# Optimization experiments

Measured on AMD Instinct MI355X. Metric: run time of the kernel, lower is better.

## Reference

```python
import jax, jax.numpy as jnp
import numpy as np

D, HS, HE, E, K = 1024, 2048, 1024, 8, 2   # d_model, shared hidden (d_ff//2), expert hidden (d_ff//4), n_experts, top_k
B, T = 4, 1024
N_SHARED = 1


def setup_inputs() -> dict:
    key = jax.random.key(0)
    ks = jax.random.split(key, 9)
    g = lambda k, shape, s: jax.random.normal(k, shape, jnp.float32) * s
    return {
        "x": g(ks[0], (B, T, D), 1.0),
        "t_emb": g(ks[1], (B, D), 1.0),
        "router_W": g(ks[2], (2 * D, E), 0.01),      # torch Linear(2C->E, bias=False), std=0.01 init
        "router_bias": jnp.zeros((E,), jnp.float32),  # load-balance bias buffer
        "w1": g(ks[3], (D, HS), 0.02),                # shared expert SwiGLU
        "w3": g(ks[4], (D, HS), 0.02),
        "w2": g(ks[5], (HS, D), 0.02),
        "W1e": g(ks[6], (E, D, HE), 0.02),            # routed experts, Linear->GELU->Linear
        "W2e": g(ks[7], (E, HE, D), 0.02),
    }


def reference(x, t_emb, router_W, router_bias, w1, w3, w2, W1e, W2e):
    Bb, Tt, C = x.shape
    xf = x.reshape(-1, C)                                              # [N, C]
    tf = jnp.broadcast_to(t_emb[:, None, :], (Bb, Tt, C)).reshape(-1, C)
    N = xf.shape[0]

    shared = (jax.nn.silu(xf @ w1) * (xf @ w3)) @ w2                   # [N, C]

    # router affinity (sigmoid, fp32)
    s = jax.nn.sigmoid((jnp.concatenate([xf, tf], axis=-1) @ router_W).astype(jnp.float32))
    sel_scores = s + router_bias                                       # [N, E]
    _, topk_idx = jax.lax.top_k(sel_scores, K)                         # [N, K]

    # gates normalized over selected raw affinities
    s_sel = jnp.take_along_axis(s, topk_idx, axis=1)                   # [N, K]
    denom = s_sel.sum(axis=1, keepdims=True)
    gates = jnp.where(denom > 1e-9, s_sel / (denom + 1e-9), 1.0 / K).astype(x.dtype)

    # combine weights [N, E]: scatter gates to selected experts
    combine = jnp.zeros((N, E), x.dtype).at[jnp.arange(N)[:, None], topk_idx].add(gates)

    # dense expert evaluation (reference form of grouped GEMM + scatter-combine)
    h = jax.nn.gelu(jnp.einsum('nc,ech->enh', xf, W1e), approximate=False)  # [E, N, He]
    y = jnp.einsum('enh,ehc->enc', h, W2e)                                   # [E, N, C]
    routed = jnp.einsum('ne,enc->nc', combine, y)                            # [N, C]

    return ((shared + routed) / (N_SHARED + K)).reshape(Bb, Tt, C)
```

## Files before the change

### kernel.cpp

```cpp
#include <hip/hip_runtime.h>
#include <hip/hip_bf16.h>
#include <math.h>

#define D_MODEL 1024
#define HS 2048
#define HE 1024
#define NEXP 8
#define NTOK 4096
#define NSLOT 8192

typedef __attribute__((ext_vector_type(4))) float f32x4;
typedef __attribute__((ext_vector_type(8))) short bf16x8;

__device__ __forceinline__ short f2b(float f) {
  __hip_bfloat16 h = __float2bfloat16(f);
  return *reinterpret_cast<short*>(&h);
}
__device__ __forceinline__ float b2f(short s) {
  return __bfloat162float(*reinterpret_cast<__hip_bfloat16*>(&s));
}

__device__ __forceinline__ void gl_lds16(const short* g, short* l) {
  __builtin_amdgcn_global_load_lds(
      (const __attribute__((address_space(1))) void*)g,
      (__attribute__((address_space(3))) void*)l, 16, 0, 0);
}

__device__ __forceinline__ void tr_tile(const float* __restrict__ in,
                                        short* __restrict__ out, int R, int C,
                                        int bx, int by, int bz, int rmap,
                                        float (*tile)[69], int t) {
  const int c0 = bx * 64;
  const int r0 = by * 64;
  const size_t bo = (size_t)bz * R * C;
  const int lr = t >> 4;
  const int lc4 = (t & 15) * 4;
#pragma unroll
  for (int i = 0; i < 4; i++) {
    const float4 v = *(const float4*)&in[bo + (size_t)(r0 + lr + i * 16) * C + c0 + lc4];
    tile[lc4 + 0][lr + i * 16] = v.x;
    tile[lc4 + 1][lr + i * 16] = v.y;
    tile[lc4 + 2][lr + i * 16] = v.z;
    tile[lc4 + 3][lr + i * 16] = v.w;
  }
  __syncthreads();
#pragma unroll
  for (int i = 0; i < 4; i++) {
    const int oc = (t >> 4) + i * 16;
    const int or4 = (t & 15) * 4;
    short4 o;
    o.x = f2b(tile[oc][or4 + 0]);
    o.y = f2b(tile[oc][or4 + 1]);
    o.z = f2b(tile[oc][or4 + 2]);
    o.w = f2b(tile[oc][or4 + 3]);
    const int c = c0 + oc;
    size_t orow;
    if (rmap == 0) orow = bo + (size_t)c * R;
    else orow = (size_t)((c >> 5) * 64 + (rmap == 2 ? 32 : 0) + (c & 31)) * R;
    *(short4*)&out[orow + r0 + or4] = o;
  }
}

__global__ __launch_bounds__(256) void tr_w13(const float* __restrict__ w1,
                                              const float* __restrict__ w3,
                                              short* __restrict__ w13I) {
  __shared__ float tile[64][69];
  const int z = blockIdx.z;
  tr_tile(z ? w3 : w1, w13I, D_MODEL, HS, blockIdx.x, blockIdx.y, 0, z ? 2 : 1,
          tile, threadIdx.x);
}

__global__ __launch_bounds__(256) void tr_w2(const float* __restrict__ w2,
                                             short* __restrict__ w2T) {
  __shared__ float tile[64][69];
  tr_tile(w2, w2T, HS, D_MODEL, blockIdx.x, blockIdx.y, 0, 0, tile, threadIdx.x);
}

__global__ __launch_bounds__(256) void tr_exp(const float* __restrict__ W1e,
                                              const float* __restrict__ W2e,
                                              short* __restrict__ W1eT,
                                              short* __restrict__ W2eT) {
  __shared__ float tile[64][69];
  const int z = blockIdx.z;
  if (z < 8)
    tr_tile(W1e, W1eT, D_MODEL, HE, blockIdx.x, blockIdx.y, z, 0, tile, threadIdx.x);
  else
    tr_tile(W2e, W2eT, HE, D_MODEL, blockIdx.x, blockIdx.y, z - 8, 0, tile, threadIdx.x);
}

__global__ __launch_bounds__(256) void router_kernel(
    const float* __restrict__ x, const float* __restrict__ temb,
    const float* __restrict__ rw, const float* __restrict__ rbias,
    short* __restrict__ xb, int* __restrict__ topk, float* __restrict__ gates) {
  const int t = (blockIdx.x * 256 + threadIdx.x) >> 6;
  const int lane = threadIdx.x & 63;
  const float* xr = x + (size_t)t * D_MODEL;
  const float* tr = temb + (size_t)(t >> 10) * D_MODEL;
  float acc[NEXP] = {};
#pragma unroll
  for (int i = 0; i < 4; i++) {
    const int j = i * 256 + lane * 4;
    const float4 xv = *(const float4*)&xr[j];
    const float4 tv = *(const float4*)&tr[j];
    short4 o;
    o.x = f2b(xv.x); o.y = f2b(xv.y); o.z = f2b(xv.z); o.w = f2b(xv.w);
    *(short4*)&xb[(size_t)t * D_MODEL + j] = o;
    const float* wx = rw + (size_t)j * NEXP;
    const float* wt = rw + (size_t)(D_MODEL + j) * NEXP;
    const float xa[4] = {xv.x, xv.y, xv.z, xv.w};
    const float ta[4] = {tv.x, tv.y, tv.z, tv.w};
#pragma unroll
    for (int u = 0; u < 4; u++)
#pragma unroll
      for (int e = 0; e < NEXP; e++)
        acc[e] += xa[u] * wx[u * NEXP + e] + ta[u] * wt[u * NEXP + e];
  }
#pragma unroll
  for (int off = 32; off; off >>= 1)
#pragma unroll
    for (int e = 0; e < NEXP; e++) acc[e] += __shfl_xor(acc[e], off);
  if (lane == 0) {
    float s[NEXP], sel[NEXP];
#pragma unroll
    for (int e = 0; e < NEXP; e++) {
      s[e] = 1.f / (1.f + expf(-acc[e]));
      sel[e] = s[e] + rbias[e];
    }
    int i0 = 0;
#pragma unroll
    for (int e = 1; e < NEXP; e++) if (sel[e] > sel[i0]) i0 = e;
    int i1 = (i0 == 0) ? 1 : 0;
#pragma unroll
    for (int e = 0; e < NEXP; e++) if (e != i0 && sel[e] > sel[i1]) i1 = e;
    float s0 = s[i0], s1 = s[i1], den = s0 + s1;
    float g0, g1;
    if (den > 1e-9f) { g0 = s0 / (den + 1e-9f); g1 = s1 / (den + 1e-9f); }
    else { g0 = 0.5f; g1 = 0.5f; }
    topk[t * 2] = i0; topk[t * 2 + 1] = i1;
    gates[t * 2] = g0; gates[t * 2 + 1] = g1;
  }
}

__global__ __launch_bounds__(1024) void group_kernel(const int* __restrict__ topk,
                                                     int* __restrict__ perm,
                                                     int* __restrict__ offs,
                                                     int* __restrict__ te,
                                                     int* __restrict__ tm,
                                                     int* __restrict__ ntile) {
  __shared__ int cnt[NEXP], cur[NEXP];
  const int t = threadIdx.x;
  if (t < NEXP) cnt[t] = 0;
  __syncthreads();
  int mye[8];
#pragma unroll
  for (int i = 0; i < 8; i++) {
    mye[i] = topk[i * 1024 + t];
    atomicAdd(&cnt[mye[i]], 1);
  }
  __syncthreads();
  if (t == 0) {
    int a = 0;
    for (int e = 0; e < NEXP; e++) { offs[e] = a; cur[e] = a; a += cnt[e]; }
    offs[NEXP] = a;
    int nt = 0;
    for (int e = 0; e < NEXP; e++)
      for (int m0 = 0; m0 < cnt[e]; m0 += 256) { te[nt] = e; tm[nt] = m0; nt++; }
    ntile[0] = nt;
  }
  __syncthreads();
#pragma unroll
  for (int i = 0; i < 8; i++) {
    int pos = atomicAdd(&cur[mye[i]], 1);
    perm[pos] = i * 1024 + t;
  }
}

template <int MODE>
__global__ __launch_bounds__(512, 1) void moe_gemm_ct(
    const short* __restrict__ A, const short* __restrict__ B, short* __restrict__ Cout,
    const int* __restrict__ perm, const int* __restrict__ offs,
    const float* __restrict__ gates, const int* __restrict__ te,
    const int* __restrict__ tm, const int* __restrict__ ntile) {
  extern __shared__ short lds[];
  const int td = threadIdx.x;
  int bx, m0, rbeg = 0, rend = 0;
  const short* Bbase;
  if (MODE == 0) {
    const int id = blockIdx.x, xcd = id & 7, slot = id >> 3;
    bx = (xcd & 3) * 4 + (slot & 3);
    m0 = ((xcd >> 2) * 8 + (slot >> 2)) * 256;
    Bbase = B + (size_t)bx * 256 * 1024;
  } else {
    const int id = blockIdx.x;
    const int work = (id & 7) * 20 + (id >> 3);
    const int ty = work >> 2;
    if (ty >= ntile[0]) return;
    bx = work & 3;
    const int e = te[ty];
    m0 = tm[ty];
    rbeg = offs[e]; rend = offs[e + 1];
    Bbase = B + ((size_t)e * 1024 + bx * 256) * 1024;
  }

  const int srow = td >> 3;
  const int colsw8 = ((td & 7) ^ (srow & 7)) * 8;
  const short* ap[2][2];
  const short* bp[2][2];
#pragma unroll
  for (int h = 0; h < 2; h++)
#pragma unroll
    for (int i = 0; i < 2; i++) {
      const int trow = h * 128 + i * 64 + srow;
      int grow;
      if (MODE == 0) grow = m0 + trow;
      else if (MODE == 1) grow = perm[min(rbeg + m0 + trow, rend - 1)] >> 1;
      else grow = min(rbeg + m0 + trow, rend - 1);
      ap[h][i] = A + (size_t)grow * 1024 + colsw8;
      bp[h][i] = Bbase + (size_t)trow * 1024 + colsw8;
    }

#define STAGE_ALL(t_, b_)                                                       \
  do {                                                                          \
    gl_lds16(bp[0][0] + (t_) * 64, lds + (b_) * 32768 + 16384 + td * 8);        \
    gl_lds16(bp[0][1] + (t_) * 64, lds + (b_) * 32768 + 16384 + 4096 + td * 8); \
    gl_lds16(bp[1][0] + (t_) * 64, lds + (b_) * 32768 + 16384 + 8192 + td * 8); \
    gl_lds16(bp[1][1] + (t_) * 64, lds + (b_) * 32768 + 16384 + 12288 + td * 8);\
    gl_lds16(ap[0][0] + (t_) * 64, lds + (b_) * 32768 + td * 8);                \
    gl_lds16(ap[0][1] + (t_) * 64, lds + (b_) * 32768 + 4096 + td * 8);         \
    gl_lds16(ap[1][0] + (t_) * 64, lds + (b_) * 32768 + 8192 + td * 8);         \
    gl_lds16(ap[1][1] + (t_) * 64, lds + (b_) * 32768 + 12288 + td * 8);        \
  } while (0)

  const int l = td & 63;
  const int wid = td >> 6;
  const int mh = wid >> 2;
  const int wn4 = wid & 3;
  const int lr = l & 15;
  const int bhsel = wn4 >> 1;
  const int bnr = (wn4 & 1) * 64;
  const int swzk0 = ((0 + (l >> 4) * 16) ^ ((l & 7) << 4)) >> 1;
  const int swzk1 = ((64 + (l >> 4) * 16) ^ ((l & 7) << 4)) >> 1;

#define LDA(mf_, swz_) (*(const bf16x8*)&Ah[(unsigned)(((mf_)*16 + lr) * 64) + (swz_)])
#define LDB(nf_, swz_) (*(const bf16x8*)&Bh[(unsigned)((bnr + (nf_)*16 + lr) * 64) + (swz_)])
#define MMROW(mf_, a_)                                                                 \
  acc[mf_][0] = __builtin_amdgcn_mfma_f32_16x16x32_bf16(a_, b0, acc[mf_][0], 0, 0, 0); \
  acc[mf_][1] = __builtin_amdgcn_mfma_f32_16x16x32_bf16(a_, b1, acc[mf_][1], 0, 0, 0); \
  acc[mf_][2] = __builtin_amdgcn_mfma_f32_16x16x32_bf16(a_, b2, acc[mf_][2], 0, 0, 0); \
  acc[mf_][3] = __builtin_amdgcn_mfma_f32_16x16x32_bf16(a_, b3, acc[mf_][3], 0, 0, 0)

  f32x4 acc[8][4] = {};

  STAGE_ALL(0, 0);

  for (int t = 0; t < 16; ++t) {
    const int p = t & 1, q = p ^ 1;
    const short* Ah = lds + p * 32768 + mh * 8192;
    const short* Bh = lds + p * 32768 + 16384 + bhsel * 8192;
    if (t < 15) {
      STAGE_ALL(t + 1, q);
      asm volatile("s_waitcnt vmcnt(8)" ::: "memory");
    } else {
      asm volatile("s_waitcnt vmcnt(0)" ::: "memory");
    }
    __builtin_amdgcn_s_barrier();
    {
      bf16x8 b0, b1, b2, b3, a0, a1, a2, a3;
      b0 = LDB(0, swzk0); b1 = LDB(1, swzk0); b2 = LDB(2, swzk0); b3 = LDB(3, swzk0);
      a0 = LDA(0, swzk0); a1 = LDA(1, swzk0); a2 = LDA(2, swzk0); a3 = LDA(3, swzk0);
      __builtin_amdgcn_s_setprio(1);
      MMROW(0, a0); MMROW(1, a1); MMROW(2, a2); MMROW(3, a3);
      __builtin_amdgcn_s_setprio(0);
      a0 = LDA(4, swzk0); a1 = LDA(5, swzk0); a2 = LDA(6, swzk0); a3 = LDA(7, swzk0);
      __builtin_amdgcn_s_setprio(1);
      MMROW(4, a0); MMROW(5, a1); MMROW(6, a2); MMROW(7, a3);
      __builtin_amdgcn_s_setprio(0);
      b0 = LDB(0, swzk1); b1 = LDB(1, swzk1); b2 = LDB(2, swzk1); b3 = LDB(3, swzk1);
      a0 = LDA(0, swzk1); a1 = LDA(1, swzk1); a2 = LDA(2, swzk1); a3 = LDA(3, swzk1);
      __builtin_amdgcn_s_setprio(1);
      MMROW(0, a0); MMROW(1, a1); MMROW(2, a2); MMROW(3, a3);
      __builtin_amdgcn_s_setprio(0);
      a0 = LDA(4, swzk1); a1 = LDA(5, swzk1); a2 = LDA(6, swzk1); a3 = LDA(7, swzk1);
      __builtin_amdgcn_s_setprio(1);
      MMROW(4, a0); MMROW(5, a1); MMROW(6, a2); MMROW(7, a3);
      __builtin_amdgcn_s_setprio(0);
    }
    __builtin_amdgcn_sched_barrier(0);
    __builtin_amdgcn_s_barrier();
  }

  const int rsub = (l >> 4) * 4;
  if (MODE == 0) {
#pragma unroll
    for (int mf = 0; mf < 8; mf++)
#pragma unroll
      for (int j = 0; j < 4; j++) {
        const int row = m0 + mh * 128 + mf * 16 + rsub + j;
        short* Up = Cout + (size_t)row * HS + bx * 128 + wn4 * 32 + lr;
#pragma unroll
        for (int nfp = 0; nfp < 2; nfp++) {
          const float a = acc[mf][nfp][j];
          const float b = acc[mf][nfp + 2][j];
          Up[nfp * 16] = f2b(a / (1.f + expf(-a)) * b);
        }
      }
  } else if (MODE == 1) {
#pragma unroll
    for (int mf = 0; mf < 8; mf++)
#pragma unroll
      for (int j = 0; j < 4; j++) {
        const int gi = rbeg + m0 + mh * 128 + mf * 16 + rsub + j;
        if (gi < rend) {
          short* Cp = Cout + (size_t)gi * HE + bx * 256 + wn4 * 64 + lr;
#pragma unroll
          for (int nf = 0; nf < 4; nf++) {
            const float v = acc[mf][nf][j];
            Cp[nf * 16] = f2b(0.5f * v * (1.0f + erff(v * 0.70710678118654752f)));
          }
        }
      }
  } else {
#pragma unroll
    for (int mf = 0; mf < 8; mf++)
#pragma unroll
      for (int j = 0; j < 4; j++) {
        const int gi = rbeg + m0 + mh * 128 + mf * 16 + rsub + j;
        if (gi < rend) {
          const int slot = perm[gi];
          const float g = gates[slot];
          short* Cp = Cout + (size_t)slot * D_MODEL + bx * 256 + wn4 * 64 + lr;
#pragma unroll
          for (int nf = 0; nf < 4; nf++) Cp[nf * 16] = f2b(g * acc[mf][nf][j]);
        }
      }
  }
#undef STAGE_ALL
#undef LDA
#undef LDB
#undef MMROW
}

__global__ __launch_bounds__(256, 2) void gemm_g2_ct(
    const short* __restrict__ A, const short* __restrict__ B,
    const short* __restrict__ yb, float* __restrict__ out) {
  extern __shared__ short lds[];
  const int td = threadIdx.x;
  const int id = blockIdx.x, xcd = id & 7, slot = id >> 3;
  const int tile_n = (slot & 7) * 128;
  const int m0 = (xcd * 4 + (slot >> 3)) * 128;

  const int srow = td >> 3;
  const int colsw8 = ((td & 7) ^ (srow & 7)) * 8;
  const short* ap[4];
  const short* bp[4];
#pragma unroll
  for (int u = 0; u < 4; u++) {
    ap[u] = A + (size_t)(m0 + u * 32 + srow) * HS + colsw8;
    bp[u] = B + (size_t)(tile_n + u * 32 + srow) * HS + colsw8;
  }

#define STAGE_ALL2(t_, b_)                                                 \
  do {                                                                     \
    gl_lds16(ap[0] + (t_) * 64, lds + (b_) * 16384 + td * 8);              \
    gl_lds16(ap[1] + (t_) * 64, lds + (b_) * 16384 + 2048 + td * 8);       \
    gl_lds16(ap[2] + (t_) * 64, lds + (b_) * 16384 + 4096 + td * 8);       \
    gl_lds16(ap[3] + (t_) * 64, lds + (b_) * 16384 + 6144 + td * 8);       \
    gl_lds16(bp[0] + (t_) * 64, lds + (b_) * 16384 + 8192 + td * 8);       \
    gl_lds16(bp[1] + (t_) * 64, lds + (b_) * 16384 + 10240 + td * 8);      \
    gl_lds16(bp[2] + (t_) * 64, lds + (b_) * 16384 + 12288 + td * 8);      \
    gl_lds16(bp[3] + (t_) * 64, lds + (b_) * 16384 + 14336 + td * 8);      \
  } while (0)

  const int l = td & 63;
  const int wv = td >> 6;
  const int wm = (wv >> 1) * 64, wn = (wv & 1) * 64;
  const int lr = l & 15;
  const int swzk0 = ((0 + (l >> 4) * 16) ^ ((l & 7) << 4)) >> 1;
  const int swzk1 = ((64 + (l >> 4) * 16) ^ ((l & 7) << 4)) >> 1;

#define LDA2(mf_, swz_) (*(const bf16x8*)&Ah[(unsigned)(((mf_)*16 + lr) * 64) + (swz_)])
#define LDB2(nf_, swz_) (*(const bf16x8*)&Bh[(unsigned)(((nf_)*16 + lr) * 64) + (swz_)])
#define MMROW2(mf_, a_)                                                                \
  acc[mf_][0] = __builtin_amdgcn_mfma_f32_16x16x32_bf16(a_, b0, acc[mf_][0], 0, 0, 0); \
  acc[mf_][1] = __builtin_amdgcn_mfma_f32_16x16x32_bf16(a_, b1, acc[mf_][1], 0, 0, 0); \
  acc[mf_][2] = __builtin_amdgcn_mfma_f32_16x16x32_bf16(a_, b2, acc[mf_][2], 0, 0, 0); \
  acc[mf_][3] = __builtin_amdgcn_mfma_f32_16x16x32_bf16(a_, b3, acc[mf_][3], 0, 0, 0)

  f32x4 acc[4][4] = {};

  STAGE_ALL2(0, 0);
  for (int t = 0; t < 32; ++t) {
    const int p = t & 1, q = p ^ 1;
    const short* Ah = lds + p * 16384 + wm * 64;
    const short* Bh = lds + p * 16384 + 8192 + wn * 64;
    if (t < 31) {
      STAGE_ALL2(t + 1, q);
      asm volatile("s_waitcnt vmcnt(8)" ::: "memory");
    } else {
      asm volatile("s_waitcnt vmcnt(0)" ::: "memory");
    }
    __builtin_amdgcn_s_barrier();
    {
      bf16x8 b0, b1, b2, b3, a0, a1, a2, a3;
      b0 = LDB2(0, swzk0); b1 = LDB2(1, swzk0); b2 = LDB2(2, swzk0); b3 = LDB2(3, swzk0);
      a0 = LDA2(0, swzk0); a1 = LDA2(1, swzk0); a2 = LDA2(2, swzk0); a3 = LDA2(3, swzk0);
      __builtin_amdgcn_s_setprio(1);
      MMROW2(0, a0); MMROW2(1, a1); MMROW2(2, a2); MMROW2(3, a3);
      __builtin_amdgcn_s_setprio(0);
      b0 = LDB2(0, swzk1); b1 = LDB2(1, swzk1); b2 = LDB2(2, swzk1); b3 = LDB2(3, swzk1);
      a0 = LDA2(0, swzk1); a1 = LDA2(1, swzk1); a2 = LDA2(2, swzk1); a3 = LDA2(3, swzk1);
      __builtin_amdgcn_s_setprio(1);
      MMROW2(0, a0); MMROW2(1, a1); MMROW2(2, a2); MMROW2(3, a3);
      __builtin_amdgcn_s_setprio(0);
    }
    __builtin_amdgcn_sched_barrier(0);
    __builtin_amdgcn_s_barrier();
  }

  const int rq = (l >> 4) * 4;
  const float inv3 = 1.0f / 3.0f;
#pragma unroll
  for (int m = 0; m < 4; m++) {
#pragma unroll
    for (int j = 0; j < 4; j++) {
      const int tok = m0 + wm + m * 16 + rq + j;
      const int colb = tile_n + wn + lr;
      const short* y0p = yb + (size_t)(tok * 2) * D_MODEL + colb;
      const short* y1p = yb + (size_t)(tok * 2 + 1) * D_MODEL + colb;
      float* Op = out + (size_t)tok * D_MODEL + colb;
#pragma unroll
      for (int n = 0; n < 4; n++) {
        Op[n * 16] = (acc[m][n][j] + b2f(y0p[n * 16]) + b2f(y1p[n * 16])) * inv3;
      }
    }
  }
#undef STAGE_ALL2
#undef LDA2
#undef LDB2
#undef MMROW2
}

extern "C" void kernel_launch(void* const* d_in, const int* in_sizes, int n_in,
                              void* d_out, int out_size, void* d_ws, size_t ws_size,
                              hipStream_t stream) {
  const float* x = (const float*)d_in[0];
  const float* temb = (const float*)d_in[1];
  const float* rw = (const float*)d_in[2];
  const float* rbias = (const float*)d_in[3];
  const float* w1 = (const float*)d_in[4];
  const float* w3 = (const float*)d_in[5];
  const float* w2 = (const float*)d_in[6];
  const float* W1e = (const float*)d_in[7];
  const float* W2e = (const float*)d_in[8];
  float* out = (float*)d_out;

  const size_t MB = 1ull << 20;
  char* w = (char*)d_ws;
  short* xb    = (short*)(w + 0 * MB);
  short* w13I  = (short*)(w + 8 * MB);
  short* w2T   = (short*)(w + 16 * MB);
  short* W1eT  = (short*)(w + 20 * MB);
  short* W2eT  = (short*)(w + 36 * MB);
  short* ubuf  = (short*)(w + 52 * MB);
  short* hexpb = (short*)(w + 68 * MB);
  short* yb    = (short*)(w + 84 * MB);
  float* gates = (float*)(w + 100 * MB);
  int* topk    = (int*)(w + 100 * MB + 32 * 1024);
  int* perm    = (int*)(w + 100 * MB + 64 * 1024);
  int* meta    = (int*)(w + 100 * MB + 96 * 1024);
  int* offs    = meta;
  int* te      = meta + 16;
  int* tm      = meta + 128;
  int* ntile   = meta + 256;

  hipFuncSetAttribute((const void*)&moe_gemm_ct<0>,
                      hipFuncAttributeMaxDynamicSharedMemorySize, 131072);
  hipFuncSetAttribute((const void*)&moe_gemm_ct<1>,
                      hipFuncAttributeMaxDynamicSharedMemorySize, 131072);
  hipFuncSetAttribute((const void*)&moe_gemm_ct<2>,
                      hipFuncAttributeMaxDynamicSharedMemorySize, 131072);
  hipFuncSetAttribute((const void*)&gemm_g2_ct,
                      hipFuncAttributeMaxDynamicSharedMemorySize, 65536);

  tr_w13<<<dim3(HS / 64, D_MODEL / 64, 2), 256, 0, stream>>>(w1, w3, w13I);
  tr_w2<<<dim3(D_MODEL / 64, HS / 64, 1), 256, 0, stream>>>(w2, w2T);
  tr_exp<<<dim3(16, 16, 16), 256, 0, stream>>>(W1e, W2e, W1eT, W2eT);
  router_kernel<<<NTOK / 4, 256, 0, stream>>>(x, temb, rw, rbias, xb, topk, gates);
  group_kernel<<<1, 1024, 0, stream>>>(topk, perm, offs, te, tm, ntile);

  moe_gemm_ct<0><<<256, 512, 131072, stream>>>(xb, w13I, ubuf, nullptr, nullptr,
                                               nullptr, nullptr, nullptr, nullptr);

  moe_gemm_ct<1><<<160, 512, 131072, stream>>>(xb, W1eT, hexpb, perm, offs,
                                               gates, te, tm, ntile);
  moe_gemm_ct<2><<<160, 512, 131072, stream>>>(hexpb, W2eT, yb, perm, offs,
                                               gates, te, tm, ntile);

  gemm_g2_ct<<<256, 256, 65536, stream>>>(ubuf, w2T, yb, out);
}
```

Baseline: 225.7 us.

## Switch MoE and shared GEMMs to unified 128x128 tile kernel with two blocks per CU

Replaces the 256x256-tile, 512-thread GEMM used for the shared up-projection and both routed-expert GEMMs with a templated 128x128-tile, 256-thread kernel at two blocks per CU. The down-projection kernel is folded into the same template. Expert grouping now emits 128-row tiles, which cuts padding waste on uneven expert loads and gives more blocks for better CU fill. The trade is less operand reuse per tile, so each block does more global and LDS traffic per FLOP.

```diff
diff --git a/kernel.cpp b/kernel.cpp
--- a/kernel.cpp
+++ b/kernel.cpp
@@ -164,7 +164,7 @@
     offs[NEXP] = a;
     int nt = 0;
     for (int e = 0; e < NEXP; e++)
-      for (int m0 = 0; m0 < cnt[e]; m0 += 256) { te[nt] = e; tm[nt] = m0; nt++; }
+      for (int m0 = 0; m0 < cnt[e]; m0 += 128) { te[nt] = e; tm[nt] = m0; nt++; }
     ntile[0] = nt;
   }
   __syncthreads();
@@ -175,90 +175,91 @@
   }
 }
 
-template <int MODE>
-__global__ __launch_bounds__(512, 1) void moe_gemm_ct(
-    const short* __restrict__ A, const short* __restrict__ B, short* __restrict__ Cout,
+template <int MODE, int NT>
+__global__ __launch_bounds__(256, 2) void g128(
+    const short* __restrict__ A, const short* __restrict__ B, void* __restrict__ Cout,
     const int* __restrict__ perm, const int* __restrict__ offs,
     const float* __restrict__ gates, const int* __restrict__ te,
-    const int* __restrict__ tm, const int* __restrict__ ntile) {
+    const int* __restrict__ tm, const int* __restrict__ ntile,
+    const short* __restrict__ yb) {
   extern __shared__ short lds[];
   const int td = threadIdx.x;
-  int bx, m0, rbeg = 0, rend = 0;
+  const int K = NT * 64;
+
+  int m_panel = 0, n_panel = 0, e = 0, m0 = 0, rbeg = 0, rend = 0, bxn = 0;
   const short* Bbase;
   if (MODE == 0) {
-    const int id = blockIdx.x, xcd = id & 7, slot = id >> 3;
-    bx = (xcd & 3) * 4 + (slot & 3);
-    m0 = ((xcd >> 2) * 8 + (slot >> 2)) * 256;
-    Bbase = B + (size_t)bx * 256 * 1024;
+    const int xcd = blockIdx.x & 7, w = blockIdx.x >> 3;
+    n_panel = xcd * 4 + (w >> 5);
+    m_panel = w & 31;
+    Bbase = B + (size_t)n_panel * 128 * K;
+  } else if (MODE == 3) {
+    const int xcd = blockIdx.x & 7, slot = blockIdx.x >> 3;
+    n_panel = slot & 7;
+    m_panel = xcd * 4 + (slot >> 3);
+    Bbase = B + (size_t)n_panel * 128 * K;
   } else {
-    const int id = blockIdx.x;
-    const int work = (id & 7) * 20 + (id >> 3);
-    const int ty = work >> 2;
+    const int ty = blockIdx.x >> 3;
     if (ty >= ntile[0]) return;
-    bx = work & 3;
-    const int e = te[ty];
+    bxn = blockIdx.x & 7;
+    e = te[ty];
     m0 = tm[ty];
     rbeg = offs[e]; rend = offs[e + 1];
-    Bbase = B + ((size_t)e * 1024 + bx * 256) * 1024;
+    Bbase = B + ((size_t)e * 1024 + bxn * 128) * K;
   }
 
   const int srow = td >> 3;
   const int colsw8 = ((td & 7) ^ (srow & 7)) * 8;
-  const short* ap[2][2];
-  const short* bp[2][2];
-#pragma unroll
-  for (int h = 0; h < 2; h++)
-#pragma unroll
-    for (int i = 0; i < 2; i++) {
-      const int trow = h * 128 + i * 64 + srow;
-      int grow;
-      if (MODE == 0) grow = m0 + trow;
-      else if (MODE == 1) grow = perm[min(rbeg + m0 + trow, rend - 1)] >> 1;
-      else grow = min(rbeg + m0 + trow, rend - 1);
-      ap[h][i] = A + (size_t)grow * 1024 + colsw8;
-      bp[h][i] = Bbase + (size_t)trow * 1024 + colsw8;
-    }
-
-#define STAGE_ALL(t_, b_)                                                       \
-  do {                                                                          \
-    gl_lds16(bp[0][0] + (t_) * 64, lds + (b_) * 32768 + 16384 + td * 8);        \
-    gl_lds16(bp[0][1] + (t_) * 64, lds + (b_) * 32768 + 16384 + 4096 + td * 8); \
-    gl_lds16(bp[1][0] + (t_) * 64, lds + (b_) * 32768 + 16384 + 8192 + td * 8); \
-    gl_lds16(bp[1][1] + (t_) * 64, lds + (b_) * 32768 + 16384 + 12288 + td * 8);\
-    gl_lds16(ap[0][0] + (t_) * 64, lds + (b_) * 32768 + td * 8);                \
-    gl_lds16(ap[0][1] + (t_) * 64, lds + (b_) * 32768 + 4096 + td * 8);         \
-    gl_lds16(ap[1][0] + (t_) * 64, lds + (b_) * 32768 + 8192 + td * 8);         \
-    gl_lds16(ap[1][1] + (t_) * 64, lds + (b_) * 32768 + 12288 + td * 8);        \
+  const short* ap[4];
+  const short* bp[4];
+#pragma unroll
+  for (int u = 0; u < 4; u++) {
+    const int trow = u * 32 + srow;
+    int grow;
+    if (MODE == 0) grow = m_panel * 128 + trow;
+    else if (MODE == 1) grow = perm[min(rbeg + m0 + trow, rend - 1)] >> 1;
+    else if (MODE == 2) grow = min(rbeg + m0 + trow, rend - 1);
+    else grow = m_panel * 128 + trow;
+    ap[u] = A + (size_t)grow * K + colsw8;
+    bp[u] = Bbase + (size_t)trow * K + colsw8;
+  }
+
+#define STAGE(t_, b_)                                                      \
+  do {                                                                     \
+    gl_lds16(ap[0] + (t_) * 64, lds + (b_) * 16384 + td * 8);              \
+    gl_lds16(ap[1] + (t_) * 64, lds + (b_) * 16384 + 2048 + td * 8);       \
+    gl_lds16(ap[2] + (t_) * 64, lds + (b_) * 16384 + 4096 + td * 8);       \
+    gl_lds16(ap[3] + (t_) * 64, lds + (b_) * 16384 + 6144 + td * 8);       \
+    gl_lds16(bp[0] + (t_) * 64, lds + (b_) * 16384 + 8192 + td * 8);       \
+    gl_lds16(bp[1] + (t_) * 64, lds + (b_) * 16384 + 10240 + td * 8);      \
+    gl_lds16(bp[2] + (t_) * 64, lds + (b_) * 16384 + 12288 + td * 8);      \
+    gl_lds16(bp[3] + (t_) * 64, lds + (b_) * 16384 + 14336 + td * 8);      \
   } while (0)
 
   const int l = td & 63;
-  const int wid = td >> 6;
-  const int mh = wid >> 2;
-  const int wn4 = wid & 3;
+  const int wv = td >> 6;
+  const int wm = (wv >> 1) * 64, wn = (wv & 1) * 64;
   const int lr = l & 15;
-  const int bhsel = wn4 >> 1;
-  const int bnr = (wn4 & 1) * 64;
   const int swzk0 = ((0 + (l >> 4) * 16) ^ ((l & 7) << 4)) >> 1;
   const int swzk1 = ((64 + (l >> 4) * 16) ^ ((l & 7) << 4)) >> 1;
 
 #define LDA(mf_, swz_) (*(const bf16x8*)&Ah[(unsigned)(((mf_)*16 + lr) * 64) + (swz_)])
-#define LDB(nf_, swz_) (*(const bf16x8*)&Bh[(unsigned)((bnr + (nf_)*16 + lr) * 64) + (swz_)])
+#define LDB(nf_, swz_) (*(const bf16x8*)&Bh[(unsigned)(((nf_)*16 + lr) * 64) + (swz_)])
 #define MMROW(mf_, a_)                                                                 \
   acc[mf_][0] = __builtin_amdgcn_mfma_f32_16x16x32_bf16(a_, b0, acc[mf_][0], 0, 0, 0); \
   acc[mf_][1] = __builtin_amdgcn_mfma_f32_16x16x32_bf16(a_, b1, acc[mf_][1], 0, 0, 0); \
   acc[mf_][2] = __builtin_amdgcn_mfma_f32_16x16x32_bf16(a_, b2, acc[mf_][2], 0, 0, 0); \
   acc[mf_][3] = __builtin_amdgcn_mfma_f32_16x16x32_bf16(a_, b3, acc[mf_][3], 0, 0, 0)
 
-  f32x4 acc[8][4] = {};
-
-  STAGE_ALL(0, 0);
-
-  for (int t = 0; t < 16; ++t) {
+  f32x4 acc[4][4] = {};
+
+  STAGE(0, 0);
+  for (int t = 0; t < NT; ++t) {
     const int p = t & 1, q = p ^ 1;
-    const short* Ah = lds + p * 32768 + mh * 8192;
-    const short* Bh = lds + p * 32768 + 16384 + bhsel * 8192;
-    if (t < 15) {
-      STAGE_ALL(t + 1, q);
+    const short* Ah = lds + p * 16384 + wm * 64;
+    const short* Bh = lds + p * 16384 + 8192 + wn * 64;
+    if (t < NT - 1) {
+      STAGE(t + 1, q);
       asm volatile("s_waitcnt vmcnt(8)" ::: "memory");
     } else {
       asm volatile("s_waitcnt vmcnt(0)" ::: "memory");
@@ -271,47 +272,39 @@
       __builtin_amdgcn_s_setprio(1);
       MMROW(0, a0); MMROW(1, a1); MMROW(2, a2); MMROW(3, a3);
       __builtin_amdgcn_s_setprio(0);
-      a0 = LDA(4, swzk0); a1 = LDA(5, swzk0); a2 = LDA(6, swzk0); a3 = LDA(7, swzk0);
-      __builtin_amdgcn_s_setprio(1);
-      MMROW(4, a0); MMROW(5, a1); MMROW(6, a2); MMROW(7, a3);
-      __builtin_amdgcn_s_setprio(0);
       b0 = LDB(0, swzk1); b1 = LDB(1, swzk1); b2 = LDB(2, swzk1); b3 = LDB(3, swzk1);
       a0 = LDA(0, swzk1); a1 = LDA(1, swzk1); a2 = LDA(2, swzk1); a3 = LDA(3, swzk1);
       __builtin_amdgcn_s_setprio(1);
       MMROW(0, a0); MMROW(1, a1); MMROW(2, a2); MMROW(3, a3);
       __builtin_amdgcn_s_setprio(0);
-      a0 = LDA(4, swzk1); a1 = LDA(5, swzk1); a2 = LDA(6, swzk1); a3 = LDA(7, swzk1);
-      __builtin_amdgcn_s_setprio(1);
-      MMROW(4, a0); MMROW(5, a1); MMROW(6, a2); MMROW(7, a3);
-      __builtin_amdgcn_s_setprio(0);
     }
     __builtin_amdgcn_sched_barrier(0);
     __builtin_amdgcn_s_barrier();
   }
 
-  const int rsub = (l >> 4) * 4;
+  const int rq = (l >> 4) * 4;
   if (MODE == 0) {
 #pragma unroll
-    for (int mf = 0; mf < 8; mf++)
+    for (int mf = 0; mf < 4; mf++)
 #pragma unroll
       for (int j = 0; j < 4; j++) {
-        const int row = m0 + mh * 128 + mf * 16 + rsub + j;
-        short* Up = Cout + (size_t)row * HS + bx * 128 + wn4 * 32 + lr;
-#pragma unroll
-        for (int nfp = 0; nfp < 2; nfp++) {
-          const float a = acc[mf][nfp][j];
-          const float b = acc[mf][nfp + 2][j];
-          Up[nfp * 16] = f2b(a / (1.f + expf(-a)) * b);
+        const int row = m_panel * 128 + wm + mf * 16 + rq + j;
+        short* Up = (short*)Cout + (size_t)row * HS + n_panel * 64 + (wn >> 1) + lr;
+#pragma unroll
+        for (int nf = 0; nf < 2; nf++) {
+          const float a = acc[mf][nf][j];
+          const float b = acc[mf][nf + 2][j];
+          Up[nf * 16] = f2b(a / (1.f + expf(-a)) * b);
         }
       }
   } else if (MODE == 1) {
 #pragma unroll
-    for (int mf = 0; mf < 8; mf++)
+    for (int mf = 0; mf < 4; mf++)
 #pragma unroll
       for (int j = 0; j < 4; j++) {
-        const int gi = rbeg + m0 + mh * 128 + mf * 16 + rsub + j;
+        const int gi = rbeg + m0 + wm + mf * 16 + rq + j;
         if (gi < rend) {
-          short* Cp = Cout + (size_t)gi * HE + bx * 256 + wn4 * 64 + lr;
+          short* Cp = (short*)Cout + (size_t)gi * HE + bxn * 128 + wn + lr;
 #pragma unroll
           for (int nf = 0; nf < 4; nf++) {
             const float v = acc[mf][nf][j];
@@ -319,125 +312,41 @@
           }
         }
       }
-  } else {
-#pragma unroll
-    for (int mf = 0; mf < 8; mf++)
+  } else if (MODE == 2) {
+#pragma unroll
+    for (int mf = 0; mf < 4; mf++)
 #pragma unroll
       for (int j = 0; j < 4; j++) {
-        const int gi = rbeg + m0 + mh * 128 + mf * 16 + rsub + j;
+        const int gi = rbeg + m0 + wm + mf * 16 + rq + j;
         if (gi < rend) {
           const int slot = perm[gi];
           const float g = gates[slot];
-          short* Cp = Cout + (size_t)slot * D_MODEL + bx * 256 + wn4 * 64 + lr;
+          short* Cp = (short*)Cout + (size_t)slot * D_MODEL + bxn * 128 + wn + lr;
 #pragma unroll
           for (int nf = 0; nf < 4; nf++) Cp[nf * 16] = f2b(g * acc[mf][nf][j]);
         }
       }
-  }
-#undef STAGE_ALL
+  } else {
+    const float inv3 = 1.0f / 3.0f;
+#pragma unroll
+    for (int mf = 0; mf < 4; mf++)
+#pragma unroll
+      for (int j = 0; j < 4; j++) {
+        const int tok = m_panel * 128 + wm + mf * 16 + rq + j;
+        const int colb = n_panel * 128 + wn + lr;
+        const short* y0p = yb + (size_t)(tok * 2) * D_MODEL + colb;
+        const short* y1p = yb + (size_t)(tok * 2 + 1) * D_MODEL + colb;
+        float* Op = (float*)Cout + (size_t)tok * D_MODEL + colb;
+#pragma unroll
+        for (int nf = 0; nf < 4; nf++) {
+          Op[nf * 16] = (acc[mf][nf][j] + b2f(y0p[nf * 16]) + b2f(y1p[nf * 16])) * inv3;
+        }
+      }
+  }
+#undef STAGE
 #undef LDA
 #undef LDB
 #undef MMROW
-}
-
-__global__ __launch_bounds__(256, 2) void gemm_g2_ct(
-    const short* __restrict__ A, const short* __restrict__ B,
-    const short* __restrict__ yb, float* __restrict__ out) {
-  extern __shared__ short lds[];
-  const int td = threadIdx.x;
-  const int id = blockIdx.x, xcd = id & 7, slot = id >> 3;
-  const int tile_n = (slot & 7) * 128;
-  const int m0 = (xcd * 4 + (slot >> 3)) * 128;
-
-  const int srow = td >> 3;
-  const int colsw8 = ((td & 7) ^ (srow & 7)) * 8;
-  const short* ap[4];
-  const short* bp[4];
-#pragma unroll
-  for (int u = 0; u < 4; u++) {
-    ap[u] = A + (size_t)(m0 + u * 32 + srow) * HS + colsw8;
-    bp[u] = B + (size_t)(tile_n + u * 32 + srow) * HS + colsw8;
-  }
-
-#define STAGE_ALL2(t_, b_)                                                 \
-  do {                                                                     \
-    gl_lds16(ap[0] + (t_) * 64, lds + (b_) * 16384 + td * 8);              \
-    gl_lds16(ap[1] + (t_) * 64, lds + (b_) * 16384 + 2048 + td * 8);       \
-    gl_lds16(ap[2] + (t_) * 64, lds + (b_) * 16384 + 4096 + td * 8);       \
-    gl_lds16(ap[3] + (t_) * 64, lds + (b_) * 16384 + 6144 + td * 8);       \
-    gl_lds16(bp[0] + (t_) * 64, lds + (b_) * 16384 + 8192 + td * 8);       \
-    gl_lds16(bp[1] + (t_) * 64, lds + (b_) * 16384 + 10240 + td * 8);      \
-    gl_lds16(bp[2] + (t_) * 64, lds + (b_) * 16384 + 12288 + td * 8);      \
-    gl_lds16(bp[3] + (t_) * 64, lds + (b_) * 16384 + 14336 + td * 8);      \
-  } while (0)
-
-  const int l = td & 63;
-  const int wv = td >> 6;
-  const int wm = (wv >> 1) * 64, wn = (wv & 1) * 64;
-  const int lr = l & 15;
-  const int swzk0 = ((0 + (l >> 4) * 16) ^ ((l & 7) << 4)) >> 1;
-  const int swzk1 = ((64 + (l >> 4) * 16) ^ ((l & 7) << 4)) >> 1;
-
-#define LDA2(mf_, swz_) (*(const bf16x8*)&Ah[(unsigned)(((mf_)*16 + lr) * 64) + (swz_)])
-#define LDB2(nf_, swz_) (*(const bf16x8*)&Bh[(unsigned)(((nf_)*16 + lr) * 64) + (swz_)])
-#define MMROW2(mf_, a_)                                                                \
-  acc[mf_][0] = __builtin_amdgcn_mfma_f32_16x16x32_bf16(a_, b0, acc[mf_][0], 0, 0, 0); \
-  acc[mf_][1] = __builtin_amdgcn_mfma_f32_16x16x32_bf16(a_, b1, acc[mf_][1], 0, 0, 0); \
-  acc[mf_][2] = __builtin_amdgcn_mfma_f32_16x16x32_bf16(a_, b2, acc[mf_][2], 0, 0, 0); \
-  acc[mf_][3] = __builtin_amdgcn_mfma_f32_16x16x32_bf16(a_, b3, acc[mf_][3], 0, 0, 0)
-
-  f32x4 acc[4][4] = {};
-
-  STAGE_ALL2(0, 0);
-  for (int t = 0; t < 32; ++t) {
-    const int p = t & 1, q = p ^ 1;
-    const short* Ah = lds + p * 16384 + wm * 64;
-    const short* Bh = lds + p * 16384 + 8192 + wn * 64;
-    if (t < 31) {
-      STAGE_ALL2(t + 1, q);
-      asm volatile("s_waitcnt vmcnt(8)" ::: "memory");
-    } else {
-      asm volatile("s_waitcnt vmcnt(0)" ::: "memory");
-    }
-    __builtin_amdgcn_s_barrier();
-    {
-      bf16x8 b0, b1, b2, b3, a0, a1, a2, a3;
-      b0 = LDB2(0, swzk0); b1 = LDB2(1, swzk0); b2 = LDB2(2, swzk0); b3 = LDB2(3, swzk0);
-      a0 = LDA2(0, swzk0); a1 = LDA2(1, swzk0); a2 = LDA2(2, swzk0); a3 = LDA2(3, swzk0);
-      __builtin_amdgcn_s_setprio(1);
-      MMROW2(0, a0); MMROW2(1, a1); MMROW2(2, a2); MMROW2(3, a3);
-      __builtin_amdgcn_s_setprio(0);
-      b0 = LDB2(0, swzk1); b1 = LDB2(1, swzk1); b2 = LDB2(2, swzk1); b3 = LDB2(3, swzk1);
-      a0 = LDA2(0, swzk1); a1 = LDA2(1, swzk1); a2 = LDA2(2, swzk1); a3 = LDA2(3, swzk1);
-      __builtin_amdgcn_s_setprio(1);
-      MMROW2(0, a0); MMROW2(1, a1); MMROW2(2, a2); MMROW2(3, a3);
-      __builtin_amdgcn_s_setprio(0);
-    }
-    __builtin_amdgcn_sched_barrier(0);
-    __builtin_amdgcn_s_barrier();
-  }
-
-  const int rq = (l >> 4) * 4;
-  const float inv3 = 1.0f / 3.0f;
-#pragma unroll
-  for (int m = 0; m < 4; m++) {
-#pragma unroll
-    for (int j = 0; j < 4; j++) {
-      const int tok = m0 + wm + m * 16 + rq + j;
-      const int colb = tile_n + wn + lr;
-      const short* y0p = yb + (size_t)(tok * 2) * D_MODEL + colb;
-      const short* y1p = yb + (size_t)(tok * 2 + 1) * D_MODEL + colb;
-      float* Op = out + (size_t)tok * D_MODEL + colb;
-#pragma unroll
-      for (int n = 0; n < 4; n++) {
-        Op[n * 16] = (acc[m][n][j] + b2f(y0p[n * 16]) + b2f(y1p[n * 16])) * inv3;
-      }
-    }
-  }
-#undef STAGE_ALL2
-#undef LDA2
-#undef LDB2
-#undef MMROW2
 }
 
 extern "C" void kernel_launch(void* const* d_in, const int* in_sizes, int n_in,
@@ -473,13 +382,13 @@
   int* tm      = meta + 128;
   int* ntile   = meta + 256;
 
-  hipFuncSetAttribute((const void*)&moe_gemm_ct<0>,
-                      hipFuncAttributeMaxDynamicSharedMemorySize, 131072);
-  hipFuncSetAttribute((const void*)&moe_gemm_ct<1>,
-                      hipFuncAttributeMaxDynamicSharedMemorySize, 131072);
-  hipFuncSetAttribute((const void*)&moe_gemm_ct<2>,
-                      hipFuncAttributeMaxDynamicSharedMemorySize, 131072);
-  hipFuncSetAttribute((const void*)&gemm_g2_ct,
+  hipFuncSetAttribute((const void*)&g128<0, 16>,
+                      hipFuncAttributeMaxDynamicSharedMemorySize, 65536);
+  hipFuncSetAttribute((const void*)&g128<1, 16>,
+                      hipFuncAttributeMaxDynamicSharedMemorySize, 65536);
+  hipFuncSetAttribute((const void*)&g128<2, 16>,
+                      hipFuncAttributeMaxDynamicSharedMemorySize, 65536);
+  hipFuncSetAttribute((const void*)&g128<3, 32>,
                       hipFuncAttributeMaxDynamicSharedMemorySize, 65536);
 
   tr_w13<<<dim3(HS / 64, D_MODEL / 64, 2), 256, 0, stream>>>(w1, w3, w13I);
@@ -488,13 +397,14 @@
   router_kernel<<<NTOK / 4, 256, 0, stream>>>(x, temb, rw, rbias, xb, topk, gates);
   group_kernel<<<1, 1024, 0, stream>>>(topk, perm, offs, te, tm, ntile);
 
-  moe_gemm_ct<0><<<256, 512, 131072, stream>>>(xb, w13I, ubuf, nullptr, nullptr,
-                                               nullptr, nullptr, nullptr, nullptr);
-
-  moe_gemm_ct<1><<<160, 512, 131072, stream>>>(xb, W1eT, hexpb, perm, offs,
-                                               gates, te, tm, ntile);
-  moe_gemm_ct<2><<<160, 512, 131072, stream>>>(hexpb, W2eT, yb, perm, offs,
-                                               gates, te, tm, ntile);
-
-  gemm_g2_ct<<<256, 256, 65536, stream>>>(ubuf, w2T, yb, out);
-}
+  g128<0, 16><<<1024, 256, 65536, stream>>>(xb, w13I, ubuf, nullptr, nullptr,
+                                            nullptr, nullptr, nullptr, nullptr, nullptr);
+
+  g128<1, 16><<<576, 256, 65536, stream>>>(xb, W1eT, hexpb, perm, offs, gates,
+                                           te, tm, ntile, nullptr);
+  g128<2, 16><<<576, 256, 65536, stream>>>(hexpb, W2eT, yb, perm, offs, gates,
+                                           te, tm, ntile, nullptr);
+
+  g128<3, 32><<<256, 256, 65536, stream>>>(ubuf, w2T, out, nullptr, nullptr,
+                                           nullptr, nullptr, nullptr, nullptr, yb);
+}
```

Measured after the change: 225.7 us. No clear change (+0.0%).
